# Optimization experiments

Measured on AMD Instinct MI355X. Metric: run time of the kernel, lower is better.

Reference implementation:

```python
import jax, jax.numpy as jnp
import numpy as np


def _conv2d(x, w, b, pad, rhs_dilation=(1, 1)):
    out = jax.lax.conv_general_dilated(
        x, w, window_strides=(1, 1),
        padding=((pad, pad), (pad, pad)),
        rhs_dilation=rhs_dilation,
        dimension_numbers=('NCHW', 'OIHW', 'NCHW'))
    return out + b[None, :, None, None]


def _bilinear(img, gx, gy):
    # img [C,H,W]; gx,gy [9,h,w] in [-1,1]; grid_sample bilinear, align_corners=True.
    # Coords are pre-clamped to [-1,1] so all samples are in-bounds; clamped
    # neighbor indices get zero bilinear weight at the boundary, matching torch.
    C, H, W = img.shape
    ix = (gx + 1.0) * 0.5 * (W - 1)
    iy = (gy + 1.0) * 0.5 * (H - 1)
    x0 = jnp.floor(ix)
    y0 = jnp.floor(iy)
    wx = ix - x0
    wy = iy - y0
    x0i = jnp.clip(x0.astype(jnp.int32), 0, W - 1)
    x1i = jnp.clip(x0i + 1, 0, W - 1)
    y0i = jnp.clip(y0.astype(jnp.int32), 0, H - 1)
    y1i = jnp.clip(y0i + 1, 0, H - 1)
    v00 = img[:, y0i, x0i]
    v01 = img[:, y0i, x1i]
    v10 = img[:, y1i, x0i]
    v11 = img[:, y1i, x1i]
    return (v00 * (1 - wx) * (1 - wy) + v01 * wx * (1 - wy)
            + v10 * (1 - wx) * wy + v11 * wx * wy)  # [C,9,h,w]


def _forward(x, conv_w, conv_b, offset_w, offset_b, mod_w, mod_b):
    b, c, h, w = x.shape
    offset = _conv2d(x, offset_w, offset_b, pad=1)          # [b,18,h,w]
    gx = jnp.clip(offset[:, :9] + jnp.linspace(-1.0, 1.0, w)[None, None, None, :], -1.0, 1.0)
    gy = jnp.clip(offset[:, 9:] + jnp.linspace(-1.0, 1.0, h)[None, None, :, None], -1.0, 1.0)
    sampled = jax.vmap(_bilinear)(x, gx, gy)                # [b,c,9,h,w]
    mod = _conv2d(x, mod_w, mod_b, pad=1)                   # [b,9,h,w]
    interp = sampled * mod[:, None]                         # [b,c,9,h,w]
    # tile the 9 samples into a 3h x 3w spatial grid: sample k = i + j*3 goes to block (j, i)
    tiled = interp.reshape(b, c, 3, 3, h, w).transpose(0, 1, 2, 4, 3, 5).reshape(b, c, 3 * h, 3 * w)
    # dilated 3x3 conv with dilation (h+1, w+1), stride 1, padding 1 -> [b,oc,h,w]
    return _conv2d(tiled, conv_w, conv_b, pad=1, rhs_dilation=(h + 1, w + 1))


def setup_inputs() -> dict:
    key = jax.random.key(0)
    ks = jax.random.split(key, 7)
    B, C, OC, H, W = 8, 256, 256, 64, 64
    return {
        'x': jax.random.normal(ks[0], (B, C, H, W), jnp.float32),
        'conv_w': jax.random.normal(ks[1], (OC, C, 3, 3), jnp.float32) * 0.02,
        'conv_b': jax.random.normal(ks[2], (OC,), jnp.float32) * 0.02,
        'offset_w': jax.random.normal(ks[3], (18, C, 3, 3), jnp.float32) * 0.01,
        'offset_b': jax.random.normal(ks[4], (18,), jnp.float32) * 0.01,
        'mod_w': jax.random.normal(ks[5], (9, C, 3, 3), jnp.float32) * 0.02,
        'mod_b': jax.random.normal(ks[6], (9,), jnp.float32) * 0.02,
    }


def reference(x, conv_w, conv_b, offset_w, offset_b, mod_w, mod_b):
    return _forward(x, conv_w, conv_b, offset_w, offset_b, mod_w, mod_b)
```

## Files before the change

kernel.cpp:

```cpp
#include <hip/hip_runtime.h>

typedef __attribute__((ext_vector_type(8))) _Float16 f16x8;
typedef __attribute__((ext_vector_type(4))) float f32x4;

#define CB 8
#define CC 256
#define CHW 4096


__global__ __launch_bounds__(256) void prep_k(const float* __restrict__ convw,
                                              const float* __restrict__ offw,
                                              const float* __restrict__ modw,
                                              _Float16* __restrict__ wAf,
                                              _Float16* __restrict__ wAomF) {
    int i = blockIdx.x * 256 + threadIdx.x;
    {
        int lane = i & 63, tile = (i >> 6) & 15, cc = (i >> 10) & 7, t = i >> 13;
        int oc = tile * 16 + (lane & 15);
        int cb = cc * 32 + (lane >> 4) * 8;
        f16x8 v;
#pragma unroll
        for (int j = 0; j < 8; ++j)
            v[j] = (_Float16)convw[oc * 2304 + (cb + j) * 9 + t];
        *(f16x8*)(wAf + (size_t)i * 8) = v;
    }
    if (i < 9216) {
        int lane = i & 63, tile = (i >> 6) & 1, cc = (i >> 7) & 7, t = i >> 10;
        int mr = tile * 16 + (lane & 15);
        int cb = cc * 32 + (lane >> 4) * 8;
        f16x8 u;
#pragma unroll
        for (int j = 0; j < 8; ++j) {
            int c = cb + j;
            float vv = 0.f;
            if (mr < 18) vv = offw[(mr * 256 + c) * 9 + t];
            else if (mr < 27) vv = modw[((mr - 18) * 256 + c) * 9 + t];
            u[j] = (_Float16)vv;
        }
        *(f16x8*)(wAomF + (size_t)i * 8) = u;
    }
}

__global__ __launch_bounds__(256) void xk(const float* __restrict__ x,
                                          _Float16* __restrict__ xt) {
    __shared__ ushort tile[64][264];
    int bid = blockIdx.x;
    int b = bid & 7, pos0 = (bid >> 3) << 6;
    int tid = threadIdx.x;
    int p = tid & 63;
    const float* xb = x + ((size_t)b << 20);
#pragma unroll 4
    for (int rep = 0; rep < 64; rep++) {
        int c = rep * 4 + (tid >> 6);
        _Float16 h = (_Float16)xb[((size_t)c << 12) + pos0 + p];
        tile[p][c] = __builtin_bit_cast(ushort, h);
    }
    __syncthreads();
    _Float16* xtb = xt + ((size_t)b << 20);
#pragma unroll
    for (int rep = 0; rep < 8; rep++) {
        int item = rep * 256 + tid;
        int pp = item >> 5, ch = item & 31;
        f16x8 v = *(const f16x8*)((const char*)&tile[0][0] + pp * 528 + ch * 16);
        *(f16x8*)((char*)xtb + (((size_t)(pos0 + pp)) << 9) + ch * 16) = v;
    }
}

__global__ __launch_bounds__(256) void k1(const _Float16* __restrict__ xt,
                                          const _Float16* __restrict__ wAomF,
                                          const float* __restrict__ offb,
                                          const float* __restrict__ modb,
                                          float4* __restrict__ descW,
                                          int4* __restrict__ descO) {
    __shared__ float sEp[32][68];

    int bid = blockIdx.x;
    int b = bid & 7, y = bid >> 3;
    int tid = threadIdx.x;
    int lane = tid & 63;
    int w = __builtin_amdgcn_readfirstlane(tid >> 6);
    int l15 = lane & 15, oct = lane >> 4;

    const _Float16* xtb = xt + ((size_t)b << 20);
    int kylo = (y == 0) ? 1 : 0;
    int kyhi = (y == 63) ? 1 : 2;

    f32x4 acc[2];
    acc[0] = (f32x4)0.f;
    acc[1] = (f32x4)0.f;
    f16x8 Z = {};

    int px = (w << 4) + l15;

    for (int ty = kylo; ty <= kyhi; ++ty) {
        int yy = y + ty - 1;
#pragma unroll
        for (int tx = 0; tx < 3; ++tx) {
            int t = ty * 3 + tx;
            int xx = px + tx - 1;
            bool val = (xx >= 0 && xx < 64);
            int xxc = min(max(xx, 0), 63);
            const f16x8* bp = (const f16x8*)(xtb + (((yy << 6) + xxc) << 8) + oct * 8);
            const f16x8* wf = (const f16x8*)wAomF + (size_t)t * 16 * 64 + lane;
#pragma unroll
            for (int c0 = 0; c0 < 256; c0 += 32) {
                f16x8 bf = bp[c0 >> 3];
                if (!val) bf = Z;
                int cc = c0 >> 5;
#pragma unroll
                for (int m = 0; m < 2; m++) {
                    f16x8 af = wf[(cc * 2 + m) * 64];
                    acc[m] = __builtin_amdgcn_mfma_f32_16x16x32_f16(af, bf, acc[m], 0, 0, 0);
                }
            }
        }
    }

#pragma unroll
    for (int m = 0; m < 2; m++) {
#pragma unroll
        for (int r = 0; r < 4; r++) {
            int row = (m << 4) + (oct << 2) + r;
            if (row < 27) sEp[row][px] = acc[m][r];
        }
    }
    __syncthreads();

    int g = tid >> 6;
    int xx2 = tid & 63;
    if (g < 3) {
        float lx = -1.0f + xx2 * (2.0f / 63.0f);
        float ly = -1.0f + y * (2.0f / 63.0f);
#pragma unroll
        for (int j = 0; j < 3; j++) {
            int k = g * 3 + j;
            float gx = sEp[k][xx2] + offb[k] + lx;
            gx = fminf(fmaxf(gx, -1.f), 1.f);
            float gy = sEp[9 + k][xx2] + offb[9 + k] + ly;
            gy = fminf(fmaxf(gy, -1.f), 1.f);
            float m = sEp[18 + k][xx2] + modb[k];
            float ix = (gx + 1.0f) * 0.5f * 63.0f;
            float iy = (gy + 1.0f) * 0.5f * 63.0f;
            float fx = floorf(ix), fy = floorf(iy);
            float wx = ix - fx, wy = iy - fy;
            int x0 = min(max((int)fx, 0), 63);
            int x1 = min(x0 + 1, 63);
            int y0 = min(max((int)fy, 0), 63);
            int y1 = min(y0 + 1, 63);
            float w00 = (1.f - wx) * (1.f - wy) * m;
            float w01 = wx * (1.f - wy) * m;
            float w10 = (1.f - wx) * wy * m;
            float w11 = wx * wy * m;
            int di = ((b * 9 + k) << 12) + (y << 6) + xx2;
            descW[di] = make_float4(w00, w01, w10, w11);
            descO[di] = make_int4(((y0 << 6) + x0) << 9, ((y0 << 6) + x1) << 9,
                                  ((y1 << 6) + x0) << 9, ((y1 << 6) + x1) << 9);
        }
    }
}

__global__ __launch_bounds__(512, 4) void k2(const _Float16* __restrict__ xt,
                                             const _Float16* __restrict__ wAf,
                                             const float4* __restrict__ descW,
                                             const int4* __restrict__ descO,
                                             const float* __restrict__ convb,
                                             float* __restrict__ out) {
    __shared__ char cmb[2][8192];
    __shared__ float4 sDW[2][64];
    __shared__ int sDO[2][256];

    int bid = blockIdx.x;
    int b = bid & 7, oy = bid >> 3;
    int tid = threadIdx.x;
    int l = tid & 63;
    int wid = __builtin_amdgcn_readfirstlane(tid >> 6);
    int oct = l >> 4, l15 = l & 15;

    const char* xtb = (const char*)(xt + ((size_t)b << 20));

    f32x4 acc[2][4];
#pragma unroll
    for (int mt = 0; mt < 2; mt++)
#pragma unroll
        for (int nt = 0; nt < 4; nt++) acc[mt][nt] = (f32x4)0.f;

    int p_ox = (tid >> 3) & 63;
    int p_cs = tid & 7;
    int csl = (p_ox << 7) + ((p_cs ^ (p_ox & 7)) << 4);

    auto stage_desc = [&](int t) {
        int slot = t & 1;
        int xx = tid;
        int ky = t / 3, kx = t % 3;
        int yy = oy + ky - 1;
        int xp = xx + kx - 1;
        float4 w4s = make_float4(0.f, 0.f, 0.f, 0.f);
        int4 o4 = make_int4(0, 0, 0, 0);
        if (yy >= 0 && yy < 64 && xp >= 0 && xp < 64) {
            int di = ((b * 9 + t) << 12) + (yy << 6) + xp;
            w4s = descW[di];
            o4 = descO[di];
        }
        sDW[slot][xx] = w4s;
        sDO[slot][xx * 4 + 0] = o4.x;
        sDO[slot][xx * 4 + 1] = o4.y;
        sDO[slot][xx * 4 + 2] = o4.z;
        sDO[slot][xx * 4 + 3] = o4.w;
    };

    f16x8 cr[4];
    float4 w4;

    auto load_corners = [&](int t, int q) {
        int slot = t & 1;
        const int* dof = &sDO[slot][p_ox * 4];
        w4 = sDW[slot][p_ox];
#pragma unroll
        for (int c = 0; c < 4; ++c)
            cr[c] = *(const f16x8*)(xtb + dof[c] + q * 128 + p_cs * 16);
    };

    auto write_cmb = [&](int nb) {
        _Float16 h0 = (_Float16)w4.x, h1 = (_Float16)w4.y;
        _Float16 h2 = (_Float16)w4.z, h3 = (_Float16)w4.w;
        f16x8 W0 = {h0, h0, h0, h0, h0, h0, h0, h0};
        f16x8 W1 = {h1, h1, h1, h1, h1, h1, h1, h1};
        f16x8 W2 = {h2, h2, h2, h2, h2, h2, h2, h2};
        f16x8 W3 = {h3, h3, h3, h3, h3, h3, h3, h3};
        f16x8 r = cr[0] * W0 + cr[1] * W1 + cr[2] * W2 + cr[3] * W3;
        *(f16x8*)(cmb[nb] + csl) = r;
    };

    if (tid < 64) stage_desc(0);
    __syncthreads();
    load_corners(0, 0);
    write_cmb(0);
    __syncthreads();

    for (int p = 0; p < 36; ++p) {
        int t = p >> 2, q = p & 3, pb = p & 1;
        bool hasNext = (p + 1 < 36);

        f16x8 afr[2][2];
        {
            const f16x8* wf = (const f16x8*)wAf +
                              ((size_t)((t * 8 + q * 2) * 16) + wid * 2) * 64 + l;
            afr[0][0] = wf[0];
            afr[0][1] = wf[64];
            afr[1][0] = wf[16 * 64];
            afr[1][1] = wf[17 * 64];
        }

        if (hasNext) load_corners((p + 1) >> 2, (p + 1) & 3);
        if (q == 0 && t + 1 < 9 && tid < 64) stage_desc(t + 1);

        const char* src = cmb[pb];
        __builtin_amdgcn_s_setprio(1);
#pragma unroll
        for (int ks2 = 0; ks2 < 2; ++ks2) {
            f16x8 bfr[4];
            int cs = (ks2 << 2) + oct;
#pragma unroll
            for (int nt = 0; nt < 4; ++nt) {
                int ox = (nt << 4) + l15;
                bfr[nt] = *(const f16x8*)(src + (ox << 7) + ((cs ^ (ox & 7)) << 4));
            }
#pragma unroll
            for (int mt = 0; mt < 2; ++mt)
#pragma unroll
                for (int nt = 0; nt < 4; ++nt)
                    acc[mt][nt] = __builtin_amdgcn_mfma_f32_16x16x32_f16(
                        afr[ks2][mt], bfr[nt], acc[mt][nt], 0, 0, 0);
        }
        __builtin_amdgcn_s_setprio(0);

        if (hasNext) write_cmb(pb ^ 1);
        __syncthreads();
    }

    size_t outb = ((size_t)b << 20);
#pragma unroll
    for (int mt = 0; mt < 2; ++mt) {
#pragma unroll
        for (int nt = 0; nt < 4; ++nt) {
            int ox = (nt << 4) + l15;
#pragma unroll
            for (int r = 0; r < 4; ++r) {
                int oc = (wid << 5) + (mt << 4) + (oct << 2) + r;
                out[outb + (size_t)oc * 4096 + (oy << 6) + ox] = acc[mt][nt][r] + convb[oc];
            }
        }
    }
}

extern "C" void kernel_launch(void* const* d_in, const int* in_sizes, int n_in,
                              void* d_out, int out_size, void* d_ws, size_t ws_size,
                              hipStream_t stream) {
    const float* x     = (const float*)d_in[0];
    const float* convw = (const float*)d_in[1];
    const float* convb = (const float*)d_in[2];
    const float* offw  = (const float*)d_in[3];
    const float* offb  = (const float*)d_in[4];
    const float* modw  = (const float*)d_in[5];
    const float* modb  = (const float*)d_in[6];
    float* out = (float*)d_out;

    char* ws = (char*)d_ws;
    _Float16* wAf   = (_Float16*)(ws);
    _Float16* wAomF = (_Float16*)(ws + 1179648);
    float4*   descW = (float4*)(ws + 1327104);
    int4*     descO = (int4*)(ws + 6045696);
    _Float16* xt    = (_Float16*)(ws + 10764288);

    hipLaunchKernelGGL(prep_k, dim3(288), dim3(256), 0, stream, convw, offw, modw, wAf, wAomF);
    hipLaunchKernelGGL(xk, dim3(512), dim3(256), 0, stream, x, xt);
    hipLaunchKernelGGL(k1, dim3(512), dim3(256), 0, stream, xt, wAomF, offb, modb, descW, descO);
    hipLaunchKernelGGL(k2, dim3(512), dim3(512), 0, stream, xt, wAf, descW, descO, convb, out);
}
```

Measured before the change: 102.9 us.

## Split K across wave groups with 64-wide OC tiles and LDS reduction

Each wave now owns 64 output channels with four M tiles instead of 32, and the two K halves of every step are split across two groups of four waves. Partial sums are then reduced through a 32KB shared-memory buffer before the epilogue. Each wave issues half as many B-fragment LDS reads per MFMA, and descriptor offsets and fp16 weights are cached in registers once per tap instead of being reloaded every step. In exchange it doubles accumulator registers, which can hurt occupancy under launch_bounds(512,4), and adds LDS usage plus a reduction phase with extra barriers.

Measured after the change: 102.6 us. No clear change (-0.3%).

```diff
diff --git a/kernel.cpp b/kernel.cpp
--- a/kernel.cpp
+++ b/kernel.cpp
@@ -168,25 +168,30 @@
     __shared__ char cmb[2][8192];
     __shared__ float4 sDW[2][64];
     __shared__ int sDO[2][256];
+    __shared__ f32x4 sred[2048];
 
     int bid = blockIdx.x;
     int b = bid & 7, oy = bid >> 3;
     int tid = threadIdx.x;
     int l = tid & 63;
     int wid = __builtin_amdgcn_readfirstlane(tid >> 6);
+    int mgrp = wid & 3, ks = wid >> 2;
     int oct = l >> 4, l15 = l & 15;
 
     const char* xtb = (const char*)(xt + ((size_t)b << 20));
 
-    f32x4 acc[2][4];
-#pragma unroll
-    for (int mt = 0; mt < 2; mt++)
+    f32x4 acc[4][4];
+#pragma unroll
+    for (int mt = 0; mt < 4; mt++)
 #pragma unroll
         for (int nt = 0; nt < 4; nt++) acc[mt][nt] = (f32x4)0.f;
 
     int p_ox = (tid >> 3) & 63;
     int p_cs = tid & 7;
     int csl = (p_ox << 7) + ((p_cs ^ (p_ox & 7)) << 4);
+    const char* xtb_cs = xtb + p_cs * 16;
+
+    int boff = (l15 << 7) + ((((ks << 2) + oct) ^ (l15 & 7)) << 4);
 
     auto stage_desc = [&](int t) {
         int slot = t & 1;
@@ -208,32 +213,41 @@
         sDO[slot][xx * 4 + 3] = o4.w;
     };
 
-    f16x8 cr[4];
-    float4 w4;
-
-    auto load_corners = [&](int t, int q) {
+    int rdo0, rdo1, rdo2, rdo3;
+    _Float16 rh0, rh1, rh2, rh3;
+
+    auto refresh_desc = [&](int t) {
         int slot = t & 1;
         const int* dof = &sDO[slot][p_ox * 4];
-        w4 = sDW[slot][p_ox];
-#pragma unroll
-        for (int c = 0; c < 4; ++c)
-            cr[c] = *(const f16x8*)(xtb + dof[c] + q * 128 + p_cs * 16);
+        rdo0 = dof[0]; rdo1 = dof[1]; rdo2 = dof[2]; rdo3 = dof[3];
+        float4 w4 = sDW[slot][p_ox];
+        rh0 = (_Float16)w4.x; rh1 = (_Float16)w4.y;
+        rh2 = (_Float16)w4.z; rh3 = (_Float16)w4.w;
     };
 
+    f16x8 cr[4];
+
+    auto load_corners = [&](int q) {
+        const char* base = xtb_cs + (q << 7);
+        cr[0] = *(const f16x8*)(base + rdo0);
+        cr[1] = *(const f16x8*)(base + rdo1);
+        cr[2] = *(const f16x8*)(base + rdo2);
+        cr[3] = *(const f16x8*)(base + rdo3);
+    };
+
     auto write_cmb = [&](int nb) {
-        _Float16 h0 = (_Float16)w4.x, h1 = (_Float16)w4.y;
-        _Float16 h2 = (_Float16)w4.z, h3 = (_Float16)w4.w;
-        f16x8 W0 = {h0, h0, h0, h0, h0, h0, h0, h0};
-        f16x8 W1 = {h1, h1, h1, h1, h1, h1, h1, h1};
-        f16x8 W2 = {h2, h2, h2, h2, h2, h2, h2, h2};
-        f16x8 W3 = {h3, h3, h3, h3, h3, h3, h3, h3};
+        f16x8 W0 = {rh0, rh0, rh0, rh0, rh0, rh0, rh0, rh0};
+        f16x8 W1 = {rh1, rh1, rh1, rh1, rh1, rh1, rh1, rh1};
+        f16x8 W2 = {rh2, rh2, rh2, rh2, rh2, rh2, rh2, rh2};
+        f16x8 W3 = {rh3, rh3, rh3, rh3, rh3, rh3, rh3, rh3};
         f16x8 r = cr[0] * W0 + cr[1] * W1 + cr[2] * W2 + cr[3] * W3;
         *(f16x8*)(cmb[nb] + csl) = r;
     };
 
     if (tid < 64) stage_desc(0);
     __syncthreads();
-    load_corners(0, 0);
+    refresh_desc(0);
+    load_corners(0);
     write_cmb(0);
     __syncthreads();
 
@@ -241,53 +255,79 @@
         int t = p >> 2, q = p & 3, pb = p & 1;
         bool hasNext = (p + 1 < 36);
 
-        f16x8 afr[2][2];
+        f16x8 afr[4];
         {
             const f16x8* wf = (const f16x8*)wAf +
-                              ((size_t)((t * 8 + q * 2) * 16) + wid * 2) * 64 + l;
-            afr[0][0] = wf[0];
-            afr[0][1] = wf[64];
-            afr[1][0] = wf[16 * 64];
-            afr[1][1] = wf[17 * 64];
-        }
-
-        if (hasNext) load_corners((p + 1) >> 2, (p + 1) & 3);
+                              ((size_t)((t * 8 + q * 2 + ks) * 16 + mgrp * 4)) * 64 + l;
+            afr[0] = wf[0];
+            afr[1] = wf[64];
+            afr[2] = wf[128];
+            afr[3] = wf[192];
+        }
+
+        if (hasNext) {
+            int pn = p + 1;
+            if ((pn & 3) == 0) refresh_desc(pn >> 2);
+            load_corners(pn & 3);
+        }
         if (q == 0 && t + 1 < 9 && tid < 64) stage_desc(t + 1);
 
         const char* src = cmb[pb];
         __builtin_amdgcn_s_setprio(1);
-#pragma unroll
-        for (int ks2 = 0; ks2 < 2; ++ks2) {
-            f16x8 bfr[4];
-            int cs = (ks2 << 2) + oct;
+        f16x8 bfr[4];
+#pragma unroll
+        for (int nt = 0; nt < 4; ++nt)
+            bfr[nt] = *(const f16x8*)(src + boff + (nt << 11));
+#pragma unroll
+        for (int nt = 0; nt < 4; ++nt)
+#pragma unroll
+            for (int mt = 0; mt < 4; ++mt)
+                acc[mt][nt] = __builtin_amdgcn_mfma_f32_16x16x32_f16(
+                    afr[mt], bfr[nt], acc[mt][nt], 0, 0, 0);
+        __builtin_amdgcn_s_setprio(0);
+
+        if (hasNext) write_cmb(pb ^ 1);
+        __syncthreads();
+    }
+
+#pragma unroll
+    for (int R = 0; R < 2; ++R) {
+        if (ks == 1) {
+#pragma unroll
+            for (int mtl = 0; mtl < 2; ++mtl) {
+#pragma unroll
+                for (int nt = 0; nt < 4; ++nt) {
+                    int fi = (((mgrp << 1) + mtl) << 8) + (((nt << 4) + l15) << 2) + oct;
+                    sred[fi] = acc[(R << 1) + mtl][nt];
+                }
+            }
+        }
+        __syncthreads();
+        if (ks == 0) {
+#pragma unroll
+            for (int mtl = 0; mtl < 2; ++mtl) {
+#pragma unroll
+                for (int nt = 0; nt < 4; ++nt) {
+                    int fi = (((mgrp << 1) + mtl) << 8) + (((nt << 4) + l15) << 2) + oct;
+                    acc[(R << 1) + mtl][nt] += sred[fi];
+                }
+            }
+        }
+        __syncthreads();
+    }
+
+    if (ks == 0) {
+        size_t outb = ((size_t)b << 20);
+#pragma unroll
+        for (int mt = 0; mt < 4; ++mt) {
 #pragma unroll
             for (int nt = 0; nt < 4; ++nt) {
                 int ox = (nt << 4) + l15;
-                bfr[nt] = *(const f16x8*)(src + (ox << 7) + ((cs ^ (ox & 7)) << 4));
-            }
-#pragma unroll
-            for (int mt = 0; mt < 2; ++mt)
-#pragma unroll
-                for (int nt = 0; nt < 4; ++nt)
-                    acc[mt][nt] = __builtin_amdgcn_mfma_f32_16x16x32_f16(
-                        afr[ks2][mt], bfr[nt], acc[mt][nt], 0, 0, 0);
-        }
-        __builtin_amdgcn_s_setprio(0);
-
-        if (hasNext) write_cmb(pb ^ 1);
-        __syncthreads();
-    }
-
-    size_t outb = ((size_t)b << 20);
-#pragma unroll
-    for (int mt = 0; mt < 2; ++mt) {
-#pragma unroll
-        for (int nt = 0; nt < 4; ++nt) {
-            int ox = (nt << 4) + l15;
-#pragma unroll
-            for (int r = 0; r < 4; ++r) {
-                int oc = (wid << 5) + (mt << 4) + (oct << 2) + r;
-                out[outb + (size_t)oc * 4096 + (oy << 6) + ox] = acc[mt][nt][r] + convb[oc];
+#pragma unroll
+                for (int r = 0; r < 4; ++r) {
+                    int oc = (mgrp << 6) + (mt << 4) + (oct << 2) + r;
+                    out[outb + (size_t)oc * 4096 + (oy << 6) + ox] = acc[mt][nt][r] + convb[oc];
+                }
             }
         }
     }
```
